# Performance work log

Hardware: AMD Instinct MI355X
Metric: run time of the kernel (lower is better)

The kernel has to match this reference:

```python
import jax, jax.numpy as jnp
import numpy as np

C, H, W = 3, 1280, 720
BS = 20           # block size
SF = 4            # scale factor
NH, NW = H // BS, W // BS
L = NH * NW                        # 2304 blocks


def conv2d(x, w, b, stride=1):
    y = jax.lax.conv_general_dilated(
        x, w, (stride, stride), 'VALID',
        dimension_numbers=('NCHW', 'OIHW', 'NCHW'))
    return y + b[None, :, None, None]


def edge_pad1(x):
    # replicate padding=1 (padding_mode='replicate')
    return jnp.pad(x, ((0, 0), (0, 0), (1, 1), (1, 1)), mode='edge')


def zero_pad1(x):
    return jnp.pad(x, ((0, 0), (0, 0), (1, 1), (1, 1)))


def maxpool2(x):
    return jax.lax.reduce_window(x, -jnp.inf, jax.lax.max,
                                 (1, 1, 2, 2), (1, 1, 2, 2), 'VALID')


def pixel_shuffle(x, r):
    n, crr, h, w = x.shape
    c = crr // (r * r)
    x = x.reshape(n, c, r, r, h, w)
    x = x.transpose(0, 1, 4, 2, 5, 3)  # n c h r w r
    return x.reshape(n, c, h * r, w * r)


def setup_inputs() -> dict:
    key = jax.random.key(0)
    ks = jax.random.split(key, 9)

    def winit(k, shape):
        # matches torch init: std = sqrt(2 / (out_ch * kh * kw))
        std = np.sqrt(2.0 / (shape[0] * shape[2] * shape[3]))
        return jax.random.normal(k, shape, jnp.float32) * std

    return {
        'input': jax.random.uniform(ks[0], (1, C, H, W), jnp.float32),
        # gate CNN
        'w1': winit(ks[1], (16, C, 3, 3)), 'b1': jnp.zeros((16,), jnp.float32),
        'w2': winit(ks[2], (8, 16, 3, 3)), 'b2': jnp.zeros((8,), jnp.float32),
        'w3': winit(ks[3], (1, 8, BS // 4, BS // 4)), 'b3': jnp.zeros((1,), jnp.float32),
        # light expert: 3 -> 48 conv + pixel_shuffle(4)
        'wl': winit(ks[4], (C * SF * SF, C, 3, 3)), 'bl': jnp.zeros((C * SF * SF,), jnp.float32),
        # complex expert: 3 -> 32 -> 32 -> 48 + pixel_shuffle(4)
        'wc1': winit(ks[5], (32, C, 3, 3)), 'bc1': jnp.zeros((32,), jnp.float32),
        'wc2': winit(ks[6], (32, 32, 3, 3)), 'bc2': jnp.zeros((32,), jnp.float32),
        'wc3': winit(ks[7], (C * SF * SF, 32, 3, 3)), 'bc3': jnp.zeros((C * SF * SF,), jnp.float32),
    }


def _forward(input, w1, b1, w2, b2, w3, b3, wl, bl, wc1, bc1, wc2, bc2, wc3, bc3):
    # ---- gate CNN ----
    x = maxpool2(jnp.tanh(conv2d(edge_pad1(input), w1, b1)))          # [1,16,H/2,W/2]
    x = maxpool2(conv2d(edge_pad1(x), w2, b2))                        # [1,8,H/4,W/4]
    x = conv2d(x, w3, b3, stride=BS // 4)                             # [1,1,NH,NW]
    class_vector = jax.nn.sigmoid(x.reshape(-1))                      # [L]

    # ---- unfold into non-overlapping blocks (torch.nn.Unfold order) ----
    blocks = input.reshape(C, NH, BS, NW, BS).transpose(1, 3, 0, 2, 4)
    blocks = blocks.reshape(L, C, BS, BS)                             # [L,3,20,20]

    # ---- both experts on all blocks, combine by binary mask ----
    # light expert, clamp to [0,0.6] then +0.4
    light = pixel_shuffle(conv2d(zero_pad1(blocks), wl, bl), SF)
    light = jnp.clip(light, 0.0, 0.6) + 0.4
    # complex expert, clamp to [0,1]
    h1 = jax.nn.relu(conv2d(zero_pad1(blocks), wc1, bc1))
    h2 = jax.nn.relu(conv2d(zero_pad1(h1), wc2, bc2))
    comp = pixel_shuffle(conv2d(zero_pad1(h2), wc3, bc3), SF)
    comp = jnp.clip(comp, 0.0, 1.0)

    mask = class_vector > 1.0   # faithful to source (sigmoid => always False)
    out_blocks = jnp.where(mask[:, None, None, None], comp, light)    # [L,3,80,80]

    # ---- fold blocks back into the upscaled image ----
    out = out_blocks.reshape(NH, NW, C, BS * SF, BS * SF)
    out = out.transpose(2, 0, 3, 1, 4).reshape(1, C, H * SF, W * SF)  # [1,3,5120,2880]
    return out, class_vector


def reference(input, w1, b1, w2, b2, w3, b3, wl, bl, wc1, bc1, wc2, bc2, wc3, bc3):
    return _forward(input, w1, b1, w2, b2, w3, b3, wl, bl,
                    wc1, bc1, wc2, bc2, wc3, bc3)
```

## Files before the change

### kernel.cpp

```cpp
#include <hip/hip_runtime.h>
#include <math.h>

#define CC 3
#define HH 1280
#define WW 720
#define BSZ 20
#define NHB 64
#define NWB 36
#define NBLK (NHB*NWB)
#define OUT_IMG (3*5120*2880)

#define SLAB_PITCH 84
#define SLAB_ROWS  60

union __align__(16) SMem {
  struct {
    float in_s[3][22][24];
    float w_s[48*27 + 48];
    float slab[SLAB_ROWS][SLAB_PITCH];
  } L;
  struct {
    float ins[3][26][28];
    float w1s[16*27];
    float b1s[16];
    float w2s[8*16*9];
    float b2s[8];
    float w3s[200];
    float x1s[16][12][14];
    float red[256];
    float b3s;
  } G;
};

__device__ __forceinline__ void light_body(
    SMem& sm, int l,
    const float* __restrict__ inp,
    const float* __restrict__ wl,
    const float* __restrict__ bl,
    float* __restrict__ out) {
  const int bi = l / NWB, bj = l % NWB;
  const int tid = threadIdx.x;
  float* w_s = sm.L.w_s;

  for (int i = tid; i < 3*22*24; i += 256) ((float*)sm.L.in_s)[i] = 0.0f;
  for (int i = tid; i < 48*27; i += 256) w_s[i] = wl[i];
  if (tid < 48) w_s[48*27 + tid] = bl[tid];
  __syncthreads();
  for (int i = tid; i < 300; i += 256) {
    int x4 = i % 5; int r = (i / 5) % 20; int c = i / 100;
    const float4 v = *(const float4*)&inp[(c*HH + bi*BSZ + r)*WW + bj*BSZ + 4*x4];
    float* dst = &sm.L.in_s[c][r+1][1 + 4*x4];
    dst[0] = v.x; dst[1] = v.y; dst[2] = v.z; dst[3] = v.w;
  }
  __syncthreads();

  const int row0 = bi * 80, col0 = bj * 80;

  for (int slab = 0; slab < 4; ++slab) {
    if (tid < 240) {
      const int oc = tid % 48;
      const int hl = tid / 48;
      const int h  = slab*5 + hl;
      float wr[27];
      #pragma unroll
      for (int j = 0; j < 27; ++j) wr[j] = w_s[oc*27 + j];
      float acc[20];
      const float bias = w_s[48*27 + oc];
      #pragma unroll
      for (int w = 0; w < 20; ++w) acc[w] = bias;

      #pragma unroll
      for (int ic = 0; ic < 3; ++ic)
        #pragma unroll
        for (int ky = 0; ky < 3; ++ky) {
          const float* row = &sm.L.in_s[ic][h + ky][0];
          float r[24];
          #pragma unroll
          for (int j = 0; j < 6; ++j) {
            float4 v = ((const float4*)row)[j];
            r[j*4+0] = v.x; r[j*4+1] = v.y; r[j*4+2] = v.z; r[j*4+3] = v.w;
          }
          const float w0 = wr[ic*9 + ky*3 + 0];
          const float w1 = wr[ic*9 + ky*3 + 1];
          const float w2 = wr[ic*9 + ky*3 + 2];
          #pragma unroll
          for (int w = 0; w < 20; ++w)
            acc[w] += r[w]*w0 + r[w+1]*w1 + r[w+2]*w2;
        }

      const int c  = oc >> 4;
      const int r1 = (oc >> 2) & 3;
      const int r2 = oc & 3;
      float* dst = &sm.L.slab[c*20 + hl*4 + r1][r2];
      #pragma unroll
      for (int w = 0; w < 20; ++w)
        dst[4*w] = fminf(fmaxf(acc[w], 0.0f), 0.6f) + 0.4f;
    }
    __syncthreads();

    for (int i = tid; i < SLAB_ROWS*20; i += 256) {
      const int rrow = i / 20, cb = i % 20;
      const int c = rrow / 20, lr = rrow % 20;
      const float4 v = *(const float4*)&sm.L.slab[rrow][4*cb];
      const int gy = row0 + slab*20 + lr;
      *(float4*)&out[(c*5120 + gy)*2880 + col0 + 4*cb] = v;
    }
    __syncthreads();
  }
}

__device__ __forceinline__ void gate_body(
    SMem& sm, int l,
    const float* __restrict__ inp,
    const float* __restrict__ w1,
    const float* __restrict__ b1,
    const float* __restrict__ w2,
    const float* __restrict__ b2,
    const float* __restrict__ w3,
    const float* __restrict__ b3,
    float* __restrict__ cv) {
  const int tid = threadIdx.x;
  const int oy = l / NWB, ox = l % NWB;

  for (int i = tid; i < 16*27; i += 256) sm.G.w1s[i] = w1[i];
  for (int i = tid; i < 8*16*9; i += 256) sm.G.w2s[i] = w2[i];
  for (int i = tid; i < 200; i += 256) sm.G.w3s[i] = w3[i];
  if (tid < 16) sm.G.b1s[tid] = b1[tid];
  if (tid < 8)  sm.G.b2s[tid] = b2[tid];
  if (tid == 0) sm.G.b3s = b3[0];

  for (int i = tid; i < 3*26*28; i += 256) {
    int b = i % 28; int a = (i / 28) % 26; int ic = i / (26*28);
    int gy = 20*oy - 3 + a; gy = gy < 0 ? 0 : (gy > HH-1 ? HH-1 : gy);
    int gx = 20*ox - 3 + b; gx = gx < 0 ? 0 : (gx > WW-1 ? WW-1 : gx);
    sm.G.ins[ic][a][b] = inp[(ic*HH + gy)*WW + gx];
  }
  __syncthreads();

  for (int v = tid; v < 16*12*12; v += 256) {
    int oc = v / 144; int rem = v - oc*144; int ly = rem / 12; int lx = rem - ly*12;
    int y1 = 10*oy - 1 + ly; y1 = y1 < 0 ? 0 : (y1 > 639 ? 639 : y1);
    int x1 = 10*ox - 1 + lx; x1 = x1 < 0 ? 0 : (x1 > 359 ? 359 : x1);
    int ry = 2*y1 + 2 - 20*oy;
    int rx = 2*x1 + 2 - 20*ox;
    float patch[3][4][4];
    #pragma unroll
    for (int ic = 0; ic < 3; ++ic)
      #pragma unroll
      for (int d = 0; d < 4; ++d) {
        const float2 pa = *(const float2*)&sm.G.ins[ic][ry + d][rx];
        const float2 pb = *(const float2*)&sm.G.ins[ic][ry + d][rx + 2];
        patch[ic][d][0] = pa.x; patch[ic][d][1] = pa.y;
        patch[ic][d][2] = pb.x; patch[ic][d][3] = pb.y;
      }
    float m = -1e30f;
    #pragma unroll
    for (int sy = 0; sy < 2; ++sy)
      #pragma unroll
      for (int sx = 0; sx < 2; ++sx) {
        float acc = sm.G.b1s[oc];
        #pragma unroll
        for (int ic = 0; ic < 3; ++ic)
          #pragma unroll
          for (int ky = 0; ky < 3; ++ky)
            #pragma unroll
            for (int kx = 0; kx < 3; ++kx)
              acc += patch[ic][sy+ky][sx+kx] * sm.G.w1s[(oc*3+ic)*9 + ky*3 + kx];
        m = fmaxf(m, acc);
      }
    sm.G.x1s[oc][ly][lx] = tanhf(m);
  }
  __syncthreads();

  float prod = 0.0f;
  if (tid < 200) {
    int oc2 = tid / 25; int rem = tid - oc2*25; int j = rem / 5; int i5 = rem - j*5;
    float a00 = sm.G.b2s[oc2], a01 = a00, a10 = a00, a11 = a00;
    for (int ic = 0; ic < 16; ++ic) {
      float p[4][4];
      #pragma unroll
      for (int d = 0; d < 4; ++d) {
        const float2 pa = *(const float2*)&sm.G.x1s[ic][2*j + d][2*i5];
        const float2 pb = *(const float2*)&sm.G.x1s[ic][2*j + d][2*i5 + 2];
        p[d][0] = pa.x; p[d][1] = pa.y; p[d][2] = pb.x; p[d][3] = pb.y;
      }
      #pragma unroll
      for (int ky = 0; ky < 3; ++ky)
        #pragma unroll
        for (int kx = 0; kx < 3; ++kx) {
          float wv = sm.G.w2s[((oc2*16 + ic)*3 + ky)*3 + kx];
          a00 += p[ky  ][kx  ]*wv;
          a01 += p[ky  ][kx+1]*wv;
          a10 += p[ky+1][kx  ]*wv;
          a11 += p[ky+1][kx+1]*wv;
        }
    }
    float x2 = fmaxf(fmaxf(a00, a01), fmaxf(a10, a11));
    prod = x2 * sm.G.w3s[tid];
  }
  sm.G.red[tid] = prod;
  __syncthreads();

  if (tid < 64) {
    float s = sm.G.red[tid] + sm.G.red[tid+64] + sm.G.red[tid+128] + sm.G.red[tid+192];
    #pragma unroll
    for (int off = 32; off > 0; off >>= 1) s += __shfl_down(s, off);
    if (tid == 0)
      cv[l] = 1.0f / (1.0f + expf(-(s + sm.G.b3s)));
  }
}

__global__ __launch_bounds__(256) void fused_kernel(
    const float* __restrict__ inp,
    const float* __restrict__ w1,
    const float* __restrict__ b1,
    const float* __restrict__ w2,
    const float* __restrict__ b2,
    const float* __restrict__ w3,
    const float* __restrict__ b3,
    const float* __restrict__ wl,
    const float* __restrict__ bl,
    float* __restrict__ out) {
  __shared__ SMem sm;
  const int bid = blockIdx.x;
  if (bid & 1)
    gate_body(sm, bid >> 1, inp, w1, b1, w2, b2, w3, b3, out + OUT_IMG);
  else
    light_body(sm, bid >> 1, inp, wl, bl, out);
}

extern "C" void kernel_launch(void* const* d_in, const int* in_sizes, int n_in,
                              void* d_out, int out_size, void* d_ws, size_t ws_size,
                              hipStream_t stream) {
  const float* inp = (const float*)d_in[0];
  const float* w1  = (const float*)d_in[1];
  const float* b1  = (const float*)d_in[2];
  const float* w2  = (const float*)d_in[3];
  const float* b2  = (const float*)d_in[4];
  const float* w3  = (const float*)d_in[5];
  const float* b3  = (const float*)d_in[6];
  const float* wl  = (const float*)d_in[7];
  const float* bl  = (const float*)d_in[8];

  float* out = (float*)d_out;

  hipLaunchKernelGGL(fused_kernel, dim3(2*NBLK), dim3(256), 0, stream,
                     inp, w1, b1, w2, b2, w3, b3, wl, bl, out);
}
```

Baseline: 270.5 us.

## Register-block light conv over four channels, write output directly, vectorize gate conv

Each light-expert thread now computes one input row for four output channels at once, using transposed weights so one float4 LDS read fetches them. It then writes the pixel-shuffled result straight to global memory as float4, which removes the shared slab staging and the per-slab barriers. The gate's first conv similarly computes four output channels per thread from transposed weights, and tanhf is replaced by an exp-based fast tanh. This raises register pressure (80 accumulators) and may give less coalesced global stores, since each thread writes 20 float4 to its own row.

```diff
diff --git a/kernel.cpp b/kernel.cpp
--- a/kernel.cpp
+++ b/kernel.cpp
@@ -10,18 +10,15 @@
 #define NBLK (NHB*NWB)
 #define OUT_IMG (3*5120*2880)
 
-#define SLAB_PITCH 84
-#define SLAB_ROWS  60
-
 union __align__(16) SMem {
   struct {
-    float in_s[3][22][24];
-    float w_s[48*27 + 48];
-    float slab[SLAB_ROWS][SLAB_PITCH];
+    float in_s[3][22][28];
+    float w_t[27][48];
+    float b_s[48];
   } L;
   struct {
     float ins[3][26][28];
-    float w1s[16*27];
+    float w1t[27][16];
     float b1s[16];
     float w2s[8*16*9];
     float b2s[8];
@@ -32,6 +29,13 @@
   } G;
 };
 
+__device__ __forceinline__ float fast_tanh(float x) {
+  const float ax = fabsf(x);
+  const float e = __expf(-2.0f * ax);
+  const float t = (1.0f - e) / (1.0f + e);
+  return x < 0.0f ? -t : t;
+}
+
 __device__ __forceinline__ void light_body(
     SMem& sm, int l,
     const float* __restrict__ inp,
@@ -40,11 +44,13 @@
     float* __restrict__ out) {
   const int bi = l / NWB, bj = l % NWB;
   const int tid = threadIdx.x;
-  float* w_s = sm.L.w_s;
-
-  for (int i = tid; i < 3*22*24; i += 256) ((float*)sm.L.in_s)[i] = 0.0f;
-  for (int i = tid; i < 48*27; i += 256) w_s[i] = wl[i];
-  if (tid < 48) w_s[48*27 + tid] = bl[tid];
+
+  for (int i = tid; i < 27*48; i += 256) {
+    int k = i / 48, oc = i - k*48;
+    sm.L.w_t[k][oc] = wl[oc*27 + k];
+  }
+  if (tid < 48) sm.L.b_s[tid] = bl[tid];
+  for (int i = tid; i < 3*22*28; i += 256) ((float*)sm.L.in_s)[i] = 0.0f;
   __syncthreads();
   for (int i = tid; i < 300; i += 256) {
     int x4 = i % 5; int r = (i / 5) % 20; int c = i / 100;
@@ -54,58 +60,57 @@
   }
   __syncthreads();
 
-  const int row0 = bi * 80, col0 = bj * 80;
-
-  for (int slab = 0; slab < 4; ++slab) {
-    if (tid < 240) {
-      const int oc = tid % 48;
-      const int hl = tid / 48;
-      const int h  = slab*5 + hl;
-      float wr[27];
-      #pragma unroll
-      for (int j = 0; j < 27; ++j) wr[j] = w_s[oc*27 + j];
-      float acc[20];
-      const float bias = w_s[48*27 + oc];
-      #pragma unroll
-      for (int w = 0; w < 20; ++w) acc[w] = bias;
-
-      #pragma unroll
-      for (int ic = 0; ic < 3; ++ic)
-        #pragma unroll
-        for (int ky = 0; ky < 3; ++ky) {
-          const float* row = &sm.L.in_s[ic][h + ky][0];
-          float r[24];
+  if (tid < 240) {
+    const int h   = tid % 20;
+    const int ocg = tid / 20;
+    const int c   = ocg >> 2;
+    const int r1  = ocg & 3;
+
+    float acc[4][20];
+    {
+      const float4 b4 = *(const float4*)&sm.L.b_s[4*ocg];
+      #pragma unroll
+      for (int w = 0; w < 20; ++w) {
+        acc[0][w] = b4.x; acc[1][w] = b4.y; acc[2][w] = b4.z; acc[3][w] = b4.w;
+      }
+    }
+
+    #pragma unroll
+    for (int ic = 0; ic < 3; ++ic)
+      #pragma unroll
+      for (int ky = 0; ky < 3; ++ky) {
+        const float* row = &sm.L.in_s[ic][h + ky][0];
+        float r[24];
+        #pragma unroll
+        for (int j = 0; j < 6; ++j) {
+          float4 v = ((const float4*)row)[j];
+          r[4*j+0] = v.x; r[4*j+1] = v.y; r[4*j+2] = v.z; r[4*j+3] = v.w;
+        }
+        const int kbase = (ic*3 + ky)*3;
+        #pragma unroll
+        for (int kx = 0; kx < 3; ++kx) {
+          const float4 wv = *(const float4*)&sm.L.w_t[kbase + kx][4*ocg];
           #pragma unroll
-          for (int j = 0; j < 6; ++j) {
-            float4 v = ((const float4*)row)[j];
-            r[j*4+0] = v.x; r[j*4+1] = v.y; r[j*4+2] = v.z; r[j*4+3] = v.w;
+          for (int w = 0; w < 20; ++w) {
+            acc[0][w] += r[w+kx]*wv.x;
+            acc[1][w] += r[w+kx]*wv.y;
+            acc[2][w] += r[w+kx]*wv.z;
+            acc[3][w] += r[w+kx]*wv.w;
           }
-          const float w0 = wr[ic*9 + ky*3 + 0];
-          const float w1 = wr[ic*9 + ky*3 + 1];
-          const float w2 = wr[ic*9 + ky*3 + 2];
-          #pragma unroll
-          for (int w = 0; w < 20; ++w)
-            acc[w] += r[w]*w0 + r[w+1]*w1 + r[w+2]*w2;
-        }
-
-      const int c  = oc >> 4;
-      const int r1 = (oc >> 2) & 3;
-      const int r2 = oc & 3;
-      float* dst = &sm.L.slab[c*20 + hl*4 + r1][r2];
-      #pragma unroll
-      for (int w = 0; w < 20; ++w)
-        dst[4*w] = fminf(fmaxf(acc[w], 0.0f), 0.6f) + 0.4f;
-    }
-    __syncthreads();
-
-    for (int i = tid; i < SLAB_ROWS*20; i += 256) {
-      const int rrow = i / 20, cb = i % 20;
-      const int c = rrow / 20, lr = rrow % 20;
-      const float4 v = *(const float4*)&sm.L.slab[rrow][4*cb];
-      const int gy = row0 + slab*20 + lr;
-      *(float4*)&out[(c*5120 + gy)*2880 + col0 + 4*cb] = v;
-    }
-    __syncthreads();
+        }
+      }
+
+    const int gy = bi*80 + 4*h + r1;
+    float* orow = &out[(c*5120 + gy)*2880 + bj*80];
+    #pragma unroll
+    for (int w = 0; w < 20; ++w) {
+      float4 v;
+      v.x = fminf(fmaxf(acc[0][w], 0.0f), 0.6f) + 0.4f;
+      v.y = fminf(fmaxf(acc[1][w], 0.0f), 0.6f) + 0.4f;
+      v.z = fminf(fmaxf(acc[2][w], 0.0f), 0.6f) + 0.4f;
+      v.w = fminf(fmaxf(acc[3][w], 0.0f), 0.6f) + 0.4f;
+      *(float4*)&orow[4*w] = v;
+    }
   }
 }
 
@@ -122,7 +127,10 @@
   const int tid = threadIdx.x;
   const int oy = l / NWB, ox = l % NWB;
 
-  for (int i = tid; i < 16*27; i += 256) sm.G.w1s[i] = w1[i];
+  for (int i = tid; i < 27*16; i += 256) {
+    int k = i >> 4, oc = i & 15;
+    sm.G.w1t[k][oc] = w1[oc*27 + k];
+  }
   for (int i = tid; i < 8*16*9; i += 256) sm.G.w2s[i] = w2[i];
   for (int i = tid; i < 200; i += 256) sm.G.w3s[i] = w3[i];
   if (tid < 16) sm.G.b1s[tid] = b1[tid];
@@ -137,12 +145,15 @@
   }
   __syncthreads();
 
-  for (int v = tid; v < 16*12*12; v += 256) {
-    int oc = v / 144; int rem = v - oc*144; int ly = rem / 12; int lx = rem - ly*12;
+  for (int idx = tid; idx < 4*144; idx += 256) {
+    const int ocq = idx / 144;
+    const int pos = idx - ocq*144;
+    const int ly = pos / 12, lx = pos - ly*12;
     int y1 = 10*oy - 1 + ly; y1 = y1 < 0 ? 0 : (y1 > 639 ? 639 : y1);
     int x1 = 10*ox - 1 + lx; x1 = x1 < 0 ? 0 : (x1 > 359 ? 359 : x1);
-    int ry = 2*y1 + 2 - 20*oy;
-    int rx = 2*x1 + 2 - 20*ox;
+    const int ry = 2*y1 + 2 - 20*oy;
+    const int rx = 2*x1 + 2 - 20*ox;
+
     float patch[3][4][4];
     #pragma unroll
     for (int ic = 0; ic < 3; ++ic)
@@ -153,22 +164,38 @@
         patch[ic][d][0] = pa.x; patch[ic][d][1] = pa.y;
         patch[ic][d][2] = pb.x; patch[ic][d][3] = pb.y;
       }
-    float m = -1e30f;
-    #pragma unroll
-    for (int sy = 0; sy < 2; ++sy)
-      #pragma unroll
-      for (int sx = 0; sx < 2; ++sx) {
-        float acc = sm.G.b1s[oc];
-        #pragma unroll
-        for (int ic = 0; ic < 3; ++ic)
-          #pragma unroll
-          for (int ky = 0; ky < 3; ++ky)
-            #pragma unroll
-            for (int kx = 0; kx < 3; ++kx)
-              acc += patch[ic][sy+ky][sx+kx] * sm.G.w1s[(oc*3+ic)*9 + ky*3 + kx];
-        m = fmaxf(m, acc);
-      }
-    sm.G.x1s[oc][ly][lx] = tanhf(m);
+
+    const float4 b4 = *(const float4*)&sm.G.b1s[4*ocq];
+    float a00[4], a01[4], a10[4], a11[4];
+    #pragma unroll
+    for (int q = 0; q < 4; ++q) {
+      const float bq = q == 0 ? b4.x : (q == 1 ? b4.y : (q == 2 ? b4.z : b4.w));
+      a00[q] = bq; a01[q] = bq; a10[q] = bq; a11[q] = bq;
+    }
+
+    #pragma unroll
+    for (int ic = 0; ic < 3; ++ic)
+      #pragma unroll
+      for (int ky = 0; ky < 3; ++ky)
+        #pragma unroll
+        for (int kx = 0; kx < 3; ++kx) {
+          const int k = (ic*3 + ky)*3 + kx;
+          const float4 wv = *(const float4*)&sm.G.w1t[k][4*ocq];
+          const float p00 = patch[ic][ky  ][kx  ];
+          const float p01 = patch[ic][ky  ][kx+1];
+          const float p10 = patch[ic][ky+1][kx  ];
+          const float p11 = patch[ic][ky+1][kx+1];
+          a00[0] += p00*wv.x; a00[1] += p00*wv.y; a00[2] += p00*wv.z; a00[3] += p00*wv.w;
+          a01[0] += p01*wv.x; a01[1] += p01*wv.y; a01[2] += p01*wv.z; a01[3] += p01*wv.w;
+          a10[0] += p10*wv.x; a10[1] += p10*wv.y; a10[2] += p10*wv.z; a10[3] += p10*wv.w;
+          a11[0] += p11*wv.x; a11[1] += p11*wv.y; a11[2] += p11*wv.z; a11[3] += p11*wv.w;
+        }
+
+    #pragma unroll
+    for (int q = 0; q < 4; ++q) {
+      const float m = fmaxf(fmaxf(a00[q], a01[q]), fmaxf(a10[q], a11[q]));
+      sm.G.x1s[4*ocq + q][ly][lx] = fast_tanh(m);
+    }
   }
   __syncthreads();
 
```

Measured after the change: 316.1 us. +16.8%, slower.

## Register-block gate convs over four output channels with transposed weights and fast tanh

Applied to the files above, without the earlier changes.

The gate CNN's conv1 and conv2 now compute four output channels per thread. Weights are transposed in shared memory so each tap loads a float4 covering four channels, and patch loads are reused across those channels. tanhf is replaced by an exp-based fast_tanh. The aim is fewer shared-memory loads and redundant patch fetches in the gate half of the kernel, at the cost of less thread parallelism (conv2 runs on only 50 threads), an extra barrier, and slightly different tanh accuracy.

```diff
diff --git a/kernel.cpp b/kernel.cpp
--- a/kernel.cpp
+++ b/kernel.cpp
@@ -21,9 +21,9 @@
   } L;
   struct {
     float ins[3][26][28];
-    float w1s[16*27];
+    float w1t[27][16];
     float b1s[16];
-    float w2s[8*16*9];
+    float w2t[16][9][8];
     float b2s[8];
     float w3s[200];
     float x1s[16][12][14];
@@ -31,6 +31,13 @@
     float b3s;
   } G;
 };
+
+__device__ __forceinline__ float fast_tanh(float x) {
+  const float ax = fabsf(x);
+  const float e = __expf(-2.0f * ax);
+  const float t = (1.0f - e) / (1.0f + e);
+  return x < 0.0f ? -t : t;
+}
 
 __device__ __forceinline__ void light_body(
     SMem& sm, int l,
@@ -122,8 +129,14 @@
   const int tid = threadIdx.x;
   const int oy = l / NWB, ox = l % NWB;
 
-  for (int i = tid; i < 16*27; i += 256) sm.G.w1s[i] = w1[i];
-  for (int i = tid; i < 8*16*9; i += 256) sm.G.w2s[i] = w2[i];
+  for (int i = tid; i < 27*16; i += 256) {
+    int k = i >> 4, oc = i & 15;
+    sm.G.w1t[k][oc] = w1[oc*27 + k];
+  }
+  for (int i = tid; i < 16*9*8; i += 256) {
+    int ic = i / 72; int rem = i - ic*72; int k = rem >> 3; int oc2 = rem & 7;
+    ((float*)sm.G.w2t)[i] = w2[(oc2*16 + ic)*9 + k];
+  }
   for (int i = tid; i < 200; i += 256) sm.G.w3s[i] = w3[i];
   if (tid < 16) sm.G.b1s[tid] = b1[tid];
   if (tid < 8)  sm.G.b2s[tid] = b2[tid];
@@ -137,12 +150,15 @@
   }
   __syncthreads();
 
-  for (int v = tid; v < 16*12*12; v += 256) {
-    int oc = v / 144; int rem = v - oc*144; int ly = rem / 12; int lx = rem - ly*12;
+  for (int idx = tid; idx < 4*144; idx += 256) {
+    const int ocq = idx / 144;
+    const int pos = idx - ocq*144;
+    const int ly = pos / 12, lx = pos - ly*12;
     int y1 = 10*oy - 1 + ly; y1 = y1 < 0 ? 0 : (y1 > 639 ? 639 : y1);
     int x1 = 10*ox - 1 + lx; x1 = x1 < 0 ? 0 : (x1 > 359 ? 359 : x1);
-    int ry = 2*y1 + 2 - 20*oy;
-    int rx = 2*x1 + 2 - 20*ox;
+    const int ry = 2*y1 + 2 - 20*oy;
+    const int rx = 2*x1 + 2 - 20*ox;
+
     float patch[3][4][4];
     #pragma unroll
     for (int ic = 0; ic < 3; ++ic)
@@ -153,29 +169,54 @@
         patch[ic][d][0] = pa.x; patch[ic][d][1] = pa.y;
         patch[ic][d][2] = pb.x; patch[ic][d][3] = pb.y;
       }
-    float m = -1e30f;
-    #pragma unroll
-    for (int sy = 0; sy < 2; ++sy)
-      #pragma unroll
-      for (int sx = 0; sx < 2; ++sx) {
-        float acc = sm.G.b1s[oc];
+
+    const float4 b4 = *(const float4*)&sm.G.b1s[4*ocq];
+    float a00[4], a01[4], a10[4], a11[4];
+    a00[0]=b4.x; a00[1]=b4.y; a00[2]=b4.z; a00[3]=b4.w;
+    a01[0]=b4.x; a01[1]=b4.y; a01[2]=b4.z; a01[3]=b4.w;
+    a10[0]=b4.x; a10[1]=b4.y; a10[2]=b4.z; a10[3]=b4.w;
+    a11[0]=b4.x; a11[1]=b4.y; a11[2]=b4.z; a11[3]=b4.w;
+
+    #pragma unroll
+    for (int ic = 0; ic < 3; ++ic)
+      #pragma unroll
+      for (int ky = 0; ky < 3; ++ky)
         #pragma unroll
-        for (int ic = 0; ic < 3; ++ic)
-          #pragma unroll
-          for (int ky = 0; ky < 3; ++ky)
-            #pragma unroll
-            for (int kx = 0; kx < 3; ++kx)
-              acc += patch[ic][sy+ky][sx+kx] * sm.G.w1s[(oc*3+ic)*9 + ky*3 + kx];
-        m = fmaxf(m, acc);
-      }
-    sm.G.x1s[oc][ly][lx] = tanhf(m);
-  }
-  __syncthreads();
-
-  float prod = 0.0f;
-  if (tid < 200) {
-    int oc2 = tid / 25; int rem = tid - oc2*25; int j = rem / 5; int i5 = rem - j*5;
-    float a00 = sm.G.b2s[oc2], a01 = a00, a10 = a00, a11 = a00;
+        for (int kx = 0; kx < 3; ++kx) {
+          const int k = (ic*3 + ky)*3 + kx;
+          const float4 wv = *(const float4*)&sm.G.w1t[k][4*ocq];
+          const float p00 = patch[ic][ky  ][kx  ];
+          const float p01 = patch[ic][ky  ][kx+1];
+          const float p10 = patch[ic][ky+1][kx  ];
+          const float p11 = patch[ic][ky+1][kx+1];
+          a00[0] += p00*wv.x; a00[1] += p00*wv.y; a00[2] += p00*wv.z; a00[3] += p00*wv.w;
+          a01[0] += p01*wv.x; a01[1] += p01*wv.y; a01[2] += p01*wv.z; a01[3] += p01*wv.w;
+          a10[0] += p10*wv.x; a10[1] += p10*wv.y; a10[2] += p10*wv.z; a10[3] += p10*wv.w;
+          a11[0] += p11*wv.x; a11[1] += p11*wv.y; a11[2] += p11*wv.z; a11[3] += p11*wv.w;
+        }
+
+    #pragma unroll
+    for (int q = 0; q < 4; ++q) {
+      const float m = fmaxf(fmaxf(a00[q], a01[q]), fmaxf(a10[q], a11[q]));
+      sm.G.x1s[4*ocq + q][ly][lx] = fast_tanh(m);
+    }
+  }
+  __syncthreads();
+
+  sm.G.red[tid] = 0.0f;
+  __syncthreads();
+  if (tid < 50) {
+    const int q   = tid / 25;
+    const int win = tid - q*25;
+    const int j = win / 5, i5 = win - j*5;
+
+    const float4 b4 = *(const float4*)&sm.G.b2s[4*q];
+    float a00[4], a01[4], a10[4], a11[4];
+    a00[0]=b4.x; a00[1]=b4.y; a00[2]=b4.z; a00[3]=b4.w;
+    a01[0]=b4.x; a01[1]=b4.y; a01[2]=b4.z; a01[3]=b4.w;
+    a10[0]=b4.x; a10[1]=b4.y; a10[2]=b4.z; a10[3]=b4.w;
+    a11[0]=b4.x; a11[1]=b4.y; a11[2]=b4.z; a11[3]=b4.w;
+
     for (int ic = 0; ic < 16; ++ic) {
       float p[4][4];
       #pragma unroll
@@ -188,17 +229,24 @@
       for (int ky = 0; ky < 3; ++ky)
         #pragma unroll
         for (int kx = 0; kx < 3; ++kx) {
-          float wv = sm.G.w2s[((oc2*16 + ic)*3 + ky)*3 + kx];
-          a00 += p[ky  ][kx  ]*wv;
-          a01 += p[ky  ][kx+1]*wv;
-          a10 += p[ky+1][kx  ]*wv;
-          a11 += p[ky+1][kx+1]*wv;
+          const float4 wv = *(const float4*)&sm.G.w2t[ic][ky*3 + kx][4*q];
+          const float p00 = p[ky  ][kx  ];
+          const float p01 = p[ky  ][kx+1];
+          const float p10 = p[ky+1][kx  ];
+          const float p11 = p[ky+1][kx+1];
+          a00[0] += p00*wv.x; a00[1] += p00*wv.y; a00[2] += p00*wv.z; a00[3] += p00*wv.w;
+          a01[0] += p01*wv.x; a01[1] += p01*wv.y; a01[2] += p01*wv.z; a01[3] += p01*wv.w;
+          a10[0] += p10*wv.x; a10[1] += p10*wv.y; a10[2] += p10*wv.z; a10[3] += p10*wv.w;
+          a11[0] += p11*wv.x; a11[1] += p11*wv.y; a11[2] += p11*wv.z; a11[3] += p11*wv.w;
         }
     }
-    float x2 = fmaxf(fmaxf(a00, a01), fmaxf(a10, a11));
-    prod = x2 * sm.G.w3s[tid];
-  }
-  sm.G.red[tid] = prod;
+    #pragma unroll
+    for (int qq = 0; qq < 4; ++qq) {
+      const float x2 = fmaxf(fmaxf(a00[qq], a01[qq]), fmaxf(a10[qq], a11[qq]));
+      const int oc2 = 4*q + qq;
+      sm.G.red[oc2*25 + win] = x2 * sm.G.w3s[oc2*25 + win];
+    }
+  }
   __syncthreads();
 
   if (tid < 64) {
```

Measured after the change: 262.1 us. -3.1%, faster.
